# Performance work log

Hardware: AMD Instinct MI355X
Metric: run time of the kernel (lower is better)

Reference implementation:

```python
import jax, jax.numpy as jnp
import numpy as np
from jax import lax

B, V_ECC, V_ERR, T, C = 8192, 16, 12, 25, 32
F_IN = C * T           # 800 = temporal_out * tf_num
G = 64                 # gcn_out
H2 = 256               # hidden_size * 2
EHR_DIM, EHR_OUT = 64, 64

def _lhat(V):
    # bidirectional ring graph; PyG ChebConv sym-norm with lambda_max=2.0:
    # L_hat = (2/lmax) * (I - D^-1/2 A D^-1/2) - I = -D^-1/2 A D^-1/2
    i = np.arange(V)
    src = np.concatenate([i, (i + 1) % V])
    dst = np.concatenate([(i + 1) % V, i])
    A = np.zeros((V, V), np.float32)
    A[src, dst] = 1.0
    deg = A.sum(1)
    dinv = np.where(deg > 0, deg ** -0.5, 0.0).astype(np.float32)
    return jnp.asarray(-(dinv[:, None] * A * dinv[None, :]))

LHAT_ECC = _lhat(V_ECC)
LHAT_ERR = _lhat(V_ERR)

def setup_inputs():
    key = jax.random.key(0)
    ks = jax.random.split(key, 23)
    n = lambda k, s: jax.random.normal(k, s, jnp.float32) * 0.02
    return {
        "ecc": jax.random.normal(ks[0], (B, V_ECC, T), jnp.float32),
        "err": jax.random.normal(ks[1], (B, V_ERR, T), jnp.float32),
        "ehr": jax.random.normal(ks[2], (B, EHR_DIM), jnp.float32),
        "wt_ecc": n(ks[3], (C, 1, 3)), "bt_ecc": n(ks[4], (C,)),
        "wt_err": n(ks[5], (C, 1, 3)), "bt_err": n(ks[6], (C,)),
        "W0_ecc": n(ks[7], (F_IN, G)), "W1_ecc": n(ks[8], (F_IN, G)), "b_ecc": n(ks[9], (G,)),
        "W0_err": n(ks[10], (F_IN, G)), "W1_err": n(ks[11], (F_IN, G)), "b_err": n(ks[12], (G,)),
        "Wp_ecc": n(ks[13], (V_ECC * G, H2)), "bp_ecc": n(ks[14], (H2,)),
        "Wp_err": n(ks[15], (V_ERR * G, H2)), "bp_err": n(ks[16], (H2,)),
        "Wa": n(ks[17], (H2, 1)), "ba": n(ks[18], (1,)),
        "We": n(ks[19], (EHR_DIM, EHR_OUT)), "be": n(ks[20], (EHR_OUT,)),
        "Wf2": n(ks[21], (H2 + EHR_OUT, 1)), "bf2": n(ks[22], (1,)),
    }

def _temporal(x, w, b):
    # x: [B, V, T]; Conv1d(1 -> C, k=3, padding=1) per node, then flatten (C, T)
    bb, v, t = x.shape
    y = lax.conv_general_dilated(x.reshape(bb * v, 1, t), w, (1,), "SAME",
                                 dimension_numbers=("NCH", "OIH", "NCH"))
    y = y + b[None, :, None]
    return y.reshape(bb, v, -1)        # [B, V, C*T]

def _cheb(x, lhat, w0, w1, b):
    # K=2 ChebConv: out = T0(x)@W0 + T1(x)@W1 + b, T1 = L_hat x (batched over B)
    tx1 = jnp.einsum("uv,bvd->bud", lhat, x)
    return x @ w0 + tx1 @ w1 + b

def reference(ecc, err, ehr, wt_ecc, bt_ecc, wt_err, bt_err,
              W0_ecc, W1_ecc, b_ecc, W0_err, W1_err, b_err,
              Wp_ecc, bp_ecc, Wp_err, bp_err, Wa, ba, We, be, Wf2, bf2):
    bsz = ecc.shape[0]
    ecc_f = _temporal(ecc, wt_ecc, bt_ecc)                    # [B,16,800]
    err_f = _temporal(err, wt_err, bt_err)                    # [B,12,800]
    ecc_out = _cheb(ecc_f, LHAT_ECC, W0_ecc, W1_ecc, b_ecc)   # [B,16,64]
    err_out = _cheb(err_f, LHAT_ERR, W0_err, W1_err, b_err)   # [B,12,64]
    ecc_g = ecc_out.reshape(bsz, -1) @ Wp_ecc + bp_ecc        # [B,256]
    err_g = err_out.reshape(bsz, -1) @ Wp_err + bp_err        # [B,256]
    attn = jax.nn.sigmoid(jnp.tanh(ecc_g + err_g) @ Wa + ba)  # [B,1]
    fused = attn * ecc_g + (1.0 - attn) * err_g
    ehr_p = jax.nn.relu(ehr @ We + be)                        # dropout = identity (eval)
    combined = jnp.concatenate([fused, ehr_p], axis=1)        # [B,320]
    x = jax.nn.relu(combined)
    return jax.nn.sigmoid(x @ Wf2 + bf2)                      # [B,1]
```

## Files before the change

### kernel.cpp

```cpp
#include <hip/hip_runtime.h>
#include <math.h>

#define B_TOT 8192
#define KE 400
#define KR 300
#define MEP 416
#define MRP 320

#define ROWS 16

#define SXE_LD 424
#define SXR_LD 328
#define SEH_LD 72

#define OFF_WEFF0E 0
#define OFF_WEFF1E 1600
#define OFF_WEFF0R 3200
#define OFF_WEFF1R 4800
#define OFF_CVE    6400
#define OFF_CVR    6464
#define OFF_BE     6528
#define OFF_BR     6784
#define U_AET 14080
#define U_ART (U_AET + 256 * MEP)
#define U_WET (U_ART + 256 * MRP)

typedef __attribute__((ext_vector_type(8))) short short8;
typedef __attribute__((ext_vector_type(4))) float floatx4;

__device__ __forceinline__ float sigmoidf_(float x) { return 1.f / (1.f + __expf(-x)); }
__device__ __forceinline__ float tanhf_(float x) { float e = __expf(2.f * x); return (e - 1.f) / (e + 1.f); }
__device__ __forceinline__ unsigned short f2bf(float x) {
    unsigned u = __float_as_uint(x);
    u += 0x7fffu + ((u >> 16) & 1u);
    return (unsigned short)(u >> 16);
}

__global__ __launch_bounds__(256) void fold_temporal(
    const float* __restrict__ wt_ecc, const float* __restrict__ bt_ecc,
    const float* __restrict__ wt_err, const float* __restrict__ bt_err,
    const float* __restrict__ W0_ecc, const float* __restrict__ W1_ecc, const float* __restrict__ b_ecc,
    const float* __restrict__ W0_err, const float* __restrict__ W1_err, const float* __restrict__ b_err,
    float* __restrict__ ws)
{
    const int blk = blockIdx.x;
    const int tid = threadIdx.x;
    const int cq = tid >> 6;
    const int g  = tid & 63;

    __shared__ float red[4][64];

    if (blk < 100) {
        const int m = blk / 25;
        const int tin = blk % 25;
        const bool is_err = (m >= 2);
        const float* wt = is_err ? wt_err : wt_ecc;
        const float* W = (m & 1) ? (is_err ? W1_err : W1_ecc) : (is_err ? W0_err : W0_ecc);
        const int t0 = tin > 0 ? tin - 1 : 0;
        const int t1 = tin < 24 ? tin + 1 : 24;
        float s = 0.f;
        #pragma unroll
        for (int c8 = 0; c8 < 8; ++c8) {
            const int c = cq * 8 + c8;
            for (int t = t0; t <= t1; ++t) {
                const int k = tin - t + 1;
                s = fmaf(wt[c * 3 + k], W[(c * 25 + t) * 64 + g], s);
            }
        }
        red[cq][g] = s;
        __syncthreads();
        if (tid < 64)
            ws[m * 1600 + tin * 64 + g] = red[0][g] + red[1][g] + red[2][g] + red[3][g];
    } else if (blk < 102) {
        const bool is_err = (blk == 101);
        const float* bt = is_err ? bt_err : bt_ecc;
        const float* W0 = is_err ? W0_err : W0_ecc;
        const float* W1 = is_err ? W1_err : W1_ecc;
        const float* bb = is_err ? b_err : b_ecc;
        float s = 0.f;
        #pragma unroll
        for (int c8 = 0; c8 < 8; ++c8) {
            const int c = cq * 8 + c8;
            const float btc = bt[c];
            #pragma unroll
            for (int t = 0; t < 25; ++t) {
                const int ct = (c * 25 + t) * 64 + g;
                s = fmaf(btc, W0[ct] - W1[ct], s);
            }
        }
        red[cq][g] = s;
        __syncthreads();
        if (tid < 64)
            ws[(is_err ? OFF_CVR : OFF_CVE) + g] =
                bb[g] + red[0][g] + red[1][g] + red[2][g] + red[3][g];
    } else {
        ws[OFF_BE + tid] = 0.f;
        ws[OFF_BR + tid] = 0.f;
    }
}

__global__ __launch_bounds__(256) void fold_graph(
    const float* __restrict__ Wp_ecc, const float* __restrict__ bp_ecc,
    const float* __restrict__ Wp_err, const float* __restrict__ bp_err,
    const float* __restrict__ We,
    float* __restrict__ wsf, unsigned short* __restrict__ wsu)
{
    const int blk = blockIdx.x;
    const int h = threadIdx.x;

    if (blk < MEP) {
        const int k = blk;
        float s = 0.f;
        if (k < KE) {
            const int v = k / 25, tin = k % 25;
            const int vp = (v + 1) & 15, vm = (v + 15) & 15;
            const float* w0 = wsf + OFF_WEFF0E + tin * 64;
            const float* w1 = wsf + OFF_WEFF1E + tin * 64;
            #pragma unroll 4
            for (int g = 0; g < 64; ++g) {
                s = fmaf(w0[g], Wp_ecc[(v * 64 + g) * 256 + h], s);
                s = fmaf(-0.5f * w1[g], Wp_ecc[(vp * 64 + g) * 256 + h] + Wp_ecc[(vm * 64 + g) * 256 + h], s);
            }
        }
        wsu[U_AET + (size_t)h * MEP + k] = f2bf(s);
    } else if (blk < MEP + MRP) {
        const int k = blk - MEP;
        float s = 0.f;
        if (k < KR) {
            const int v = k / 25, tin = k % 25;
            const int vp = (v + 1) % 12, vm = (v + 11) % 12;
            const float* w0 = wsf + OFF_WEFF0R + tin * 64;
            const float* w1 = wsf + OFF_WEFF1R + tin * 64;
            #pragma unroll 4
            for (int g = 0; g < 64; ++g) {
                s = fmaf(w0[g], Wp_err[(v * 64 + g) * 256 + h], s);
                s = fmaf(-0.5f * w1[g], Wp_err[(vp * 64 + g) * 256 + h] + Wp_err[(vm * 64 + g) * 256 + h], s);
            }
        }
        wsu[U_ART + (size_t)h * MRP + k] = f2bf(s);
    } else if (blk < MEP + MRP + 16) {
        const int i = blk - (MEP + MRP);
        const float* cv = wsf + OFF_CVE;
        float s = (i == 0) ? bp_ecc[h] : 0.f;
        #pragma unroll 4
        for (int jj = 0; jj < 64; ++jj) {
            const int j = i * 64 + jj;
            s = fmaf(cv[j & 63], Wp_ecc[(size_t)j * 256 + h], s);
        }
        atomicAdd(&wsf[OFF_BE + h], s);
    } else if (blk < MEP + MRP + 32) {
        const int i = blk - (MEP + MRP + 16);
        const float* cv = wsf + OFF_CVR;
        float s = (i == 0) ? bp_err[h] : 0.f;
        if (i < 12) {
            #pragma unroll 4
            for (int jj = 0; jj < 64; ++jj) {
                const int j = i * 64 + jj;
                s = fmaf(cv[j & 63], Wp_err[(size_t)j * 256 + h], s);
            }
        }
        atomicAdd(&wsf[OFF_BR + h], s);
    } else {
        for (int it = 0; it < 16; ++it) {
            const int idx = it * 256 + h;
            const int e = idx >> 6, d = idx & 63;
            wsu[U_WET + e * 64 + d] = f2bf(We[d * 64 + e]);
        }
    }
}

__global__ __launch_bounds__(256, 3) void fused_main(
    const float* __restrict__ ecc, const float* __restrict__ err, const float* __restrict__ ehr,
    const float* __restrict__ wsf, const unsigned short* __restrict__ wsu,
    const float* __restrict__ Wa, const float* __restrict__ ba,
    const float* __restrict__ be_, const float* __restrict__ Wf2, const float* __restrict__ bf2,
    float* __restrict__ out)
{
    const unsigned short* awt_e = wsu + U_AET;
    const unsigned short* awt_r = wsu + U_ART;
    const unsigned short* wet   = wsu + U_WET;
    const float* biasE = wsf + OFF_BE;
    const float* biasR = wsf + OFF_BR;

    __shared__ __align__(16) char smem[ROWS * SXE_LD * 2 + ROWS * SXR_LD * 2 + ROWS * SEH_LD * 2];
    unsigned short* sxe = (unsigned short*)smem;
    unsigned short* sxr = sxe + ROWS * SXE_LD;
    unsigned short* seh = sxr + ROWS * SXR_LD;
    float* pa_part = (float*)smem;
    float* at_arr  = pa_part + 64;
    float* po_part = at_arr + 16;

    const int tid = threadIdx.x;
    const int row0 = blockIdx.x * ROWS;

    for (int it = 0; it < 7; ++it) {
        const int f = it * 256 + tid;
        if (f < ROWS * 106) {
            const int r = f / 106, q = f - r * 106;
            float4 v = make_float4(0.f, 0.f, 0.f, 0.f);
            if (q < 100) v = *(const float4*)(ecc + (size_t)(row0 + r) * KE + q * 4);
            const unsigned p0 = (unsigned)f2bf(v.x) | ((unsigned)f2bf(v.y) << 16);
            const unsigned p1 = (unsigned)f2bf(v.z) | ((unsigned)f2bf(v.w) << 16);
            *(uint2*)&sxe[r * SXE_LD + q * 4] = make_uint2(p0, p1);
        }
    }
    for (int it = 0; it < 6; ++it) {
        const int f = it * 256 + tid;
        if (f < ROWS * 82) {
            const int r = f / 82, q = f - r * 82;
            float4 v = make_float4(0.f, 0.f, 0.f, 0.f);
            if (q < 75) v = *(const float4*)(err + (size_t)(row0 + r) * KR + q * 4);
            const unsigned p0 = (unsigned)f2bf(v.x) | ((unsigned)f2bf(v.y) << 16);
            const unsigned p1 = (unsigned)f2bf(v.z) | ((unsigned)f2bf(v.w) << 16);
            *(uint2*)&sxr[r * SXR_LD + q * 4] = make_uint2(p0, p1);
        }
    }
    {
        const int r = tid >> 4, q = tid & 15;
        const float4 v = *(const float4*)(ehr + (size_t)(row0 + r) * 64 + q * 4);
        const unsigned p0 = (unsigned)f2bf(v.x) | ((unsigned)f2bf(v.y) << 16);
        const unsigned p1 = (unsigned)f2bf(v.z) | ((unsigned)f2bf(v.w) << 16);
        *(uint2*)&seh[r * SEH_LD + q * 4] = make_uint2(p0, p1);
    }
    __syncthreads();

    const int wv = tid >> 6, lane = tid & 63;
    const int lm = lane & 15, lq = lane >> 4;
    const int n0 = wv * 64;

    floatx4 accE[4], accR[4], accH;
    accH = (floatx4){0.f, 0.f, 0.f, 0.f};
    #pragma unroll
    for (int nt = 0; nt < 4; ++nt) {
        accE[nt] = (floatx4){0.f, 0.f, 0.f, 0.f};
        accR[nt] = (floatx4){0.f, 0.f, 0.f, 0.f};
    }

    #pragma unroll
    for (int kc = 0; kc < 2; ++kc) {
        const short8 b = *(const short8*)(wet + (wv * 16 + lm) * 64 + kc * 32 + lq * 8);
        const short8 a = *(const short8*)&seh[lm * SEH_LD + kc * 32 + lq * 8];
        accH = __builtin_amdgcn_mfma_f32_16x16x32_bf16(a, b, accH, 0, 0, 0);
    }
    #pragma unroll
    for (int kc = 0; kc < 13; ++kc) {
        const short8 a0 = *(const short8*)&sxe[lm * SXE_LD + kc * 32 + lq * 8];
        #pragma unroll
        for (int nt = 0; nt < 4; ++nt) {
            const short8 b = *(const short8*)(awt_e + (size_t)(n0 + nt * 16 + lm) * MEP + kc * 32 + lq * 8);
            accE[nt] = __builtin_amdgcn_mfma_f32_16x16x32_bf16(a0, b, accE[nt], 0, 0, 0);
        }
    }
    #pragma unroll
    for (int kc = 0; kc < 10; ++kc) {
        const short8 a0 = *(const short8*)&sxr[lm * SXR_LD + kc * 32 + lq * 8];
        #pragma unroll
        for (int nt = 0; nt < 4; ++nt) {
            const short8 b = *(const short8*)(awt_r + (size_t)(n0 + nt * 16 + lm) * MRP + kc * 32 + lq * 8);
            accR[nt] = __builtin_amdgcn_mfma_f32_16x16x32_bf16(a0, b, accR[nt], 0, 0, 0);
        }
    }

    float bE[4], bR[4], wa[4], wf[4];
    #pragma unroll
    for (int nt = 0; nt < 4; ++nt) {
        const int h = n0 + nt * 16 + lm;
        bE[nt] = biasE[h]; bR[nt] = biasR[h]; wa[nt] = Wa[h]; wf[nt] = Wf2[h];
    }
    const int e_lane = wv * 16 + lm;
    const float eh_be = be_[e_lane];
    const float eh_wf = Wf2[256 + e_lane];

    float pa_lane[4];
    #pragma unroll
    for (int rg = 0; rg < 4; ++rg) {
        float s = 0.f;
        #pragma unroll
        for (int nt = 0; nt < 4; ++nt) {
            const float ev = accE[nt][rg] + bE[nt];
            const float rv = accR[nt][rg] + bR[nt];
            s = fmaf(tanhf_(ev + rv), wa[nt], s);
        }
        s += __shfl_xor(s, 1, 64); s += __shfl_xor(s, 2, 64);
        s += __shfl_xor(s, 4, 64); s += __shfl_xor(s, 8, 64);
        pa_lane[rg] = s;
    }

    __syncthreads();
    if (lm == 0) {
        #pragma unroll
        for (int rg = 0; rg < 4; ++rg)
            pa_part[wv * 16 + lq * 4 + rg] = pa_lane[rg];
    }
    __syncthreads();
    if (tid < 16)
        at_arr[tid] = sigmoidf_(pa_part[tid] + pa_part[16 + tid] + pa_part[32 + tid] + pa_part[48 + tid] + ba[0]);
    __syncthreads();

    float po_lane[4];
    #pragma unroll
    for (int rg = 0; rg < 4; ++rg) {
        const int r = lq * 4 + rg;
        const float at = at_arr[r];
        const float om = 1.f - at;
        float s = 0.f;
        #pragma unroll
        for (int nt = 0; nt < 4; ++nt) {
            const float ev = accE[nt][rg] + bE[nt];
            const float rv = accR[nt][rg] + bR[nt];
            s = fmaf(fmaxf(at * ev + om * rv, 0.f), wf[nt], s);
        }
        s = fmaf(fmaxf(accH[rg] + eh_be, 0.f), eh_wf, s);
        s += __shfl_xor(s, 1, 64); s += __shfl_xor(s, 2, 64);
        s += __shfl_xor(s, 4, 64); s += __shfl_xor(s, 8, 64);
        po_lane[rg] = s;
    }
    if (lm == 0) {
        #pragma unroll
        for (int rg = 0; rg < 4; ++rg)
            po_part[wv * 16 + lq * 4 + rg] = po_lane[rg];
    }
    __syncthreads();
    if (tid < 16)
        out[row0 + tid] = sigmoidf_(po_part[tid] + po_part[16 + tid] + po_part[32 + tid] + po_part[48 + tid] + bf2[0]);
}

extern "C" void kernel_launch(void* const* d_in, const int* in_sizes, int n_in,
                              void* d_out, int out_size, void* d_ws, size_t ws_size,
                              hipStream_t stream)
{
    (void)in_sizes; (void)n_in; (void)out_size; (void)ws_size;
    const float* ecc    = (const float*)d_in[0];
    const float* err    = (const float*)d_in[1];
    const float* ehr    = (const float*)d_in[2];
    const float* wt_ecc = (const float*)d_in[3];
    const float* bt_ecc = (const float*)d_in[4];
    const float* wt_err = (const float*)d_in[5];
    const float* bt_err = (const float*)d_in[6];
    const float* W0_ecc = (const float*)d_in[7];
    const float* W1_ecc = (const float*)d_in[8];
    const float* b_ecc  = (const float*)d_in[9];
    const float* W0_err = (const float*)d_in[10];
    const float* W1_err = (const float*)d_in[11];
    const float* b_err  = (const float*)d_in[12];
    const float* Wp_ecc = (const float*)d_in[13];
    const float* bp_ecc = (const float*)d_in[14];
    const float* Wp_err = (const float*)d_in[15];
    const float* bp_err = (const float*)d_in[16];
    const float* Wa     = (const float*)d_in[17];
    const float* ba     = (const float*)d_in[18];
    const float* We     = (const float*)d_in[19];
    const float* be     = (const float*)d_in[20];
    const float* Wf2    = (const float*)d_in[21];
    const float* bf2    = (const float*)d_in[22];
    float* wsf = (float*)d_ws;
    unsigned short* wsu = (unsigned short*)d_ws;
    float* out = (float*)d_out;

    fold_temporal<<<dim3(103), dim3(256), 0, stream>>>(
        wt_ecc, bt_ecc, wt_err, bt_err, W0_ecc, W1_ecc, b_ecc, W0_err, W1_err, b_err, wsf);
    fold_graph<<<dim3(MEP + MRP + 32 + 1), dim3(256), 0, stream>>>(
        Wp_ecc, bp_ecc, Wp_err, bp_err, We, wsf, wsu);
    fused_main<<<dim3(B_TOT / ROWS), dim3(256), 0, stream>>>(
        ecc, err, ehr, wsf, wsu, Wa, ba, be, Wf2, bf2, out);
}
```

Before: 147.0 us.

## Merge the two weight-folding kernels into one launch with recomputed temporal folds

Fuses fold_temporal and fold_graph into a single fold_all kernel. Each graph-fold block now recomputes its own temporal-folded W0/W1 row in shared memory, and two blocks compute the bias vectors directly instead of using atomics. This removes one kernel launch and the dependency between the two launches, at the cost of redundant temporal-fold work across blocks. It also raises fused_main's launch_bounds minimum blocks from 3 to 4, which may cap registers.

```diff
diff --git a/kernel.cpp b/kernel.cpp
--- a/kernel.cpp
+++ b/kernel.cpp
@@ -13,14 +13,8 @@
 #define SXR_LD 328
 #define SEH_LD 72
 
-#define OFF_WEFF0E 0
-#define OFF_WEFF1E 1600
-#define OFF_WEFF0R 3200
-#define OFF_WEFF1R 4800
-#define OFF_CVE    6400
-#define OFF_CVR    6464
-#define OFF_BE     6528
-#define OFF_BR     6784
+#define OFF_BE 6528
+#define OFF_BR 6784
 #define U_AET 14080
 #define U_ART (U_AET + 256 * MEP)
 #define U_WET (U_ART + 256 * MRP)
@@ -36,47 +30,35 @@
     return (unsigned short)(u >> 16);
 }
 
-__global__ __launch_bounds__(256) void fold_temporal(
+__global__ __launch_bounds__(256) void fold_all(
     const float* __restrict__ wt_ecc, const float* __restrict__ bt_ecc,
     const float* __restrict__ wt_err, const float* __restrict__ bt_err,
     const float* __restrict__ W0_ecc, const float* __restrict__ W1_ecc, const float* __restrict__ b_ecc,
     const float* __restrict__ W0_err, const float* __restrict__ W1_err, const float* __restrict__ b_err,
-    float* __restrict__ ws)
+    const float* __restrict__ Wp_ecc, const float* __restrict__ bp_ecc,
+    const float* __restrict__ Wp_err, const float* __restrict__ bp_err,
+    const float* __restrict__ We,
+    float* __restrict__ wsf, unsigned short* __restrict__ wsu)
 {
     const int blk = blockIdx.x;
     const int tid = threadIdx.x;
     const int cq = tid >> 6;
     const int g  = tid & 63;
 
-    __shared__ float red[4][64];
-
-    if (blk < 100) {
-        const int m = blk / 25;
-        const int tin = blk % 25;
-        const bool is_err = (m >= 2);
-        const float* wt = is_err ? wt_err : wt_ecc;
-        const float* W = (m & 1) ? (is_err ? W1_err : W1_ecc) : (is_err ? W0_err : W0_ecc);
-        const int t0 = tin > 0 ? tin - 1 : 0;
-        const int t1 = tin < 24 ? tin + 1 : 24;
-        float s = 0.f;
-        #pragma unroll
-        for (int c8 = 0; c8 < 8; ++c8) {
-            const int c = cq * 8 + c8;
-            for (int t = t0; t <= t1; ++t) {
-                const int k = tin - t + 1;
-                s = fmaf(wt[c * 3 + k], W[(c * 25 + t) * 64 + g], s);
-            }
-        }
-        red[cq][g] = s;
-        __syncthreads();
-        if (tid < 64)
-            ws[m * 1600 + tin * 64 + g] = red[0][g] + red[1][g] + red[2][g] + red[3][g];
-    } else if (blk < 102) {
-        const bool is_err = (blk == 101);
+    __shared__ float red0[4][64];
+    __shared__ float red1[4][64];
+    __shared__ float sw0[64];
+    __shared__ float sw1[64];
+
+    if (blk < 2) {
+        const bool is_err = (blk == 1);
         const float* bt = is_err ? bt_err : bt_ecc;
         const float* W0 = is_err ? W0_err : W0_ecc;
         const float* W1 = is_err ? W1_err : W1_ecc;
         const float* bb = is_err ? b_err : b_ecc;
+        const float* Wp = is_err ? Wp_err : Wp_ecc;
+        const float* bp = is_err ? bp_err : bp_ecc;
+        const int J = (is_err ? 12 : 16) * 64;
         float s = 0.f;
         #pragma unroll
         for (int c8 = 0; c8 < 8; ++c8) {
@@ -88,88 +70,79 @@
                 s = fmaf(btc, W0[ct] - W1[ct], s);
             }
         }
-        red[cq][g] = s;
+        red0[cq][g] = s;
         __syncthreads();
         if (tid < 64)
-            ws[(is_err ? OFF_CVR : OFF_CVE) + g] =
-                bb[g] + red[0][g] + red[1][g] + red[2][g] + red[3][g];
-    } else {
-        ws[OFF_BE + tid] = 0.f;
-        ws[OFF_BR + tid] = 0.f;
-    }
-}
-
-__global__ __launch_bounds__(256) void fold_graph(
-    const float* __restrict__ Wp_ecc, const float* __restrict__ bp_ecc,
-    const float* __restrict__ Wp_err, const float* __restrict__ bp_err,
-    const float* __restrict__ We,
-    float* __restrict__ wsf, unsigned short* __restrict__ wsu)
-{
-    const int blk = blockIdx.x;
-    const int h = threadIdx.x;
-
-    if (blk < MEP) {
-        const int k = blk;
-        float s = 0.f;
-        if (k < KE) {
-            const int v = k / 25, tin = k % 25;
-            const int vp = (v + 1) & 15, vm = (v + 15) & 15;
-            const float* w0 = wsf + OFF_WEFF0E + tin * 64;
-            const float* w1 = wsf + OFF_WEFF1E + tin * 64;
-            #pragma unroll 4
-            for (int g = 0; g < 64; ++g) {
-                s = fmaf(w0[g], Wp_ecc[(v * 64 + g) * 256 + h], s);
-                s = fmaf(-0.5f * w1[g], Wp_ecc[(vp * 64 + g) * 256 + h] + Wp_ecc[(vm * 64 + g) * 256 + h], s);
-            }
-        }
-        wsu[U_AET + (size_t)h * MEP + k] = f2bf(s);
-    } else if (blk < MEP + MRP) {
-        const int k = blk - MEP;
-        float s = 0.f;
-        if (k < KR) {
-            const int v = k / 25, tin = k % 25;
-            const int vp = (v + 1) % 12, vm = (v + 11) % 12;
-            const float* w0 = wsf + OFF_WEFF0R + tin * 64;
-            const float* w1 = wsf + OFF_WEFF1R + tin * 64;
-            #pragma unroll 4
-            for (int g = 0; g < 64; ++g) {
-                s = fmaf(w0[g], Wp_err[(v * 64 + g) * 256 + h], s);
-                s = fmaf(-0.5f * w1[g], Wp_err[(vp * 64 + g) * 256 + h] + Wp_err[(vm * 64 + g) * 256 + h], s);
-            }
-        }
-        wsu[U_ART + (size_t)h * MRP + k] = f2bf(s);
-    } else if (blk < MEP + MRP + 16) {
-        const int i = blk - (MEP + MRP);
-        const float* cv = wsf + OFF_CVE;
-        float s = (i == 0) ? bp_ecc[h] : 0.f;
-        #pragma unroll 4
-        for (int jj = 0; jj < 64; ++jj) {
-            const int j = i * 64 + jj;
-            s = fmaf(cv[j & 63], Wp_ecc[(size_t)j * 256 + h], s);
-        }
-        atomicAdd(&wsf[OFF_BE + h], s);
-    } else if (blk < MEP + MRP + 32) {
-        const int i = blk - (MEP + MRP + 16);
-        const float* cv = wsf + OFF_CVR;
-        float s = (i == 0) ? bp_err[h] : 0.f;
-        if (i < 12) {
-            #pragma unroll 4
-            for (int jj = 0; jj < 64; ++jj) {
-                const int j = i * 64 + jj;
-                s = fmaf(cv[j & 63], Wp_err[(size_t)j * 256 + h], s);
-            }
-        }
-        atomicAdd(&wsf[OFF_BR + h], s);
-    } else {
+            sw0[g] = bb[g] + red0[0][g] + red0[1][g] + red0[2][g] + red0[3][g];
+        __syncthreads();
+        const int h = tid;
+        float a0 = 0.f, a1 = 0.f, a2 = 0.f, a3 = 0.f;
+        for (int j = 0; j < J; j += 4) {
+            a0 = fmaf(sw0[(j + 0) & 63], Wp[(size_t)(j + 0) * 256 + h], a0);
+            a1 = fmaf(sw0[(j + 1) & 63], Wp[(size_t)(j + 1) * 256 + h], a1);
+            a2 = fmaf(sw0[(j + 2) & 63], Wp[(size_t)(j + 2) * 256 + h], a2);
+            a3 = fmaf(sw0[(j + 3) & 63], Wp[(size_t)(j + 3) * 256 + h], a3);
+        }
+        wsf[(is_err ? OFF_BR : OFF_BE) + h] = bp[h] + ((a0 + a1) + (a2 + a3));
+    } else if (blk == 2) {
         for (int it = 0; it < 16; ++it) {
-            const int idx = it * 256 + h;
+            const int idx = it * 256 + tid;
             const int e = idx >> 6, d = idx & 63;
             wsu[U_WET + e * 64 + d] = f2bf(We[d * 64 + e]);
         }
+    } else {
+        const int kb = blk - 3;
+        const bool is_err = (kb >= MEP);
+        const int k  = is_err ? kb - MEP : kb;
+        const int KK = is_err ? KR : KE;
+        const int MP = is_err ? MRP : MEP;
+        const float* wt = is_err ? wt_err : wt_ecc;
+        const float* W0 = is_err ? W0_err : W0_ecc;
+        const float* W1 = is_err ? W1_err : W1_ecc;
+        const float* Wp = is_err ? Wp_err : Wp_ecc;
+        const int ubase = is_err ? U_ART : U_AET;
+
+        float s = 0.f;
+        if (k < KK) {
+            const int v = k / 25, tin = k % 25;
+            const int t0 = tin > 0 ? tin - 1 : 0;
+            const int t1 = tin < 24 ? tin + 1 : 24;
+            float s0 = 0.f, s1 = 0.f;
+            #pragma unroll
+            for (int c8 = 0; c8 < 8; ++c8) {
+                const int c = cq * 8 + c8;
+                for (int t = t0; t <= t1; ++t) {
+                    const int kk = tin - t + 1;
+                    const float w = wt[c * 3 + kk];
+                    const int ct = (c * 25 + t) * 64 + g;
+                    s0 = fmaf(w, W0[ct], s0);
+                    s1 = fmaf(w, W1[ct], s1);
+                }
+            }
+            red0[cq][g] = s0;
+            red1[cq][g] = s1;
+            __syncthreads();
+            if (tid < 64)
+                sw0[g] = red0[0][g] + red0[1][g] + red0[2][g] + red0[3][g];
+            else if (tid < 128)
+                sw1[tid - 64] = red1[0][tid - 64] + red1[1][tid - 64] + red1[2][tid - 64] + red1[3][tid - 64];
+            __syncthreads();
+
+            const int nv = is_err ? 12 : 16;
+            const int vp = (v + 1) % nv;
+            const int vm = (v + nv - 1) % nv;
+            const int h = tid;
+            #pragma unroll 4
+            for (int gg = 0; gg < 64; ++gg) {
+                s = fmaf(sw0[gg], Wp[(v * 64 + gg) * 256 + h], s);
+                s = fmaf(-0.5f * sw1[gg], Wp[(vp * 64 + gg) * 256 + h] + Wp[(vm * 64 + gg) * 256 + h], s);
+            }
+        }
+        wsu[ubase + (size_t)tid * MP + k] = f2bf(s);
     }
 }
 
-__global__ __launch_bounds__(256, 3) void fused_main(
+__global__ __launch_bounds__(256, 4) void fused_main(
     const float* __restrict__ ecc, const float* __restrict__ err, const float* __restrict__ ehr,
     const float* __restrict__ wsf, const unsigned short* __restrict__ wsu,
     const float* __restrict__ Wa, const float* __restrict__ ba,
@@ -357,9 +330,9 @@
     unsigned short* wsu = (unsigned short*)d_ws;
     float* out = (float*)d_out;
 
-    fold_temporal<<<dim3(103), dim3(256), 0, stream>>>(
-        wt_ecc, bt_ecc, wt_err, bt_err, W0_ecc, W1_ecc, b_ecc, W0_err, W1_err, b_err, wsf);
-    fold_graph<<<dim3(MEP + MRP + 32 + 1), dim3(256), 0, stream>>>(
+    fold_all<<<dim3(3 + MEP + MRP), dim3(256), 0, stream>>>(
+        wt_ecc, bt_ecc, wt_err, bt_err,
+        W0_ecc, W1_ecc, b_ecc, W0_err, W1_err, b_err,
         Wp_ecc, bp_ecc, Wp_err, bp_err, We, wsf, wsu);
     fused_main<<<dim3(B_TOT / ROWS), dim3(256), 0, stream>>>(
         ecc, err, ehr, wsf, wsu, Wa, ba, be, Wf2, bf2, out);
```

Result: slower. 168.6 us (+14.7%).

## Pre-convert activations to bf16 in fold kernel and drop shared-memory staging

Applied to the files above, without the earlier changes.

Moves the fp32-to-bf16 conversion of the ecc/err/ehr inputs out of the main kernel into extra blocks of the fold_graph launch, which write padded bf16 copies to the workspace. The main kernel then loads MFMA A-operands straight from global memory, with no LDS staging and no barrier. This shrinks LDS use and removes the conversion prologue from the main kernel. The cost is an extra full write and re-read of the activations through global memory, roughly 1.3x the input bytes on top of the original read.

```diff
diff --git a/kernel.cpp b/kernel.cpp
--- a/kernel.cpp
+++ b/kernel.cpp
@@ -8,10 +8,6 @@
 #define MRP 320
 
 #define ROWS 16
-
-#define SXE_LD 424
-#define SXR_LD 328
-#define SEH_LD 72
 
 #define OFF_WEFF0E 0
 #define OFF_WEFF1E 1600
@@ -24,6 +20,14 @@
 #define U_AET 14080
 #define U_ART (U_AET + 256 * MEP)
 #define U_WET (U_ART + 256 * MRP)
+#define U_XE  (U_WET + 64 * 64)
+#define U_XR  (U_XE + 8192 * MEP)
+#define U_XH  (U_XR + 8192 * MRP)
+
+#define TCE (8192 * 52)
+#define TCR (8192 * 40)
+#define TCH (8192 * 8)
+#define CONVB 768
 
 typedef __attribute__((ext_vector_type(8))) short short8;
 typedef __attribute__((ext_vector_type(4))) float floatx4;
@@ -34,6 +38,14 @@
     unsigned u = __float_as_uint(x);
     u += 0x7fffu + ((u >> 16) & 1u);
     return (unsigned short)(u >> 16);
+}
+__device__ __forceinline__ uint4 pack8(float4 a, float4 b) {
+    uint4 r;
+    r.x = (unsigned)f2bf(a.x) | ((unsigned)f2bf(a.y) << 16);
+    r.y = (unsigned)f2bf(a.z) | ((unsigned)f2bf(a.w) << 16);
+    r.z = (unsigned)f2bf(b.x) | ((unsigned)f2bf(b.y) << 16);
+    r.w = (unsigned)f2bf(b.z) | ((unsigned)f2bf(b.w) << 16);
+    return r;
 }
 
 __global__ __launch_bounds__(256) void fold_temporal(
@@ -103,6 +115,7 @@
     const float* __restrict__ Wp_ecc, const float* __restrict__ bp_ecc,
     const float* __restrict__ Wp_err, const float* __restrict__ bp_err,
     const float* __restrict__ We,
+    const float* __restrict__ ecc, const float* __restrict__ err, const float* __restrict__ ehr,
     float* __restrict__ wsf, unsigned short* __restrict__ wsu)
 {
     const int blk = blockIdx.x;
@@ -160,17 +173,52 @@
             }
         }
         atomicAdd(&wsf[OFF_BR + h], s);
-    } else {
+    } else if (blk < MEP + MRP + 33) {
         for (int it = 0; it < 16; ++it) {
             const int idx = it * 256 + h;
             const int e = idx >> 6, d = idx & 63;
             wsu[U_WET + e * 64 + d] = f2bf(We[d * 64 + e]);
         }
+    } else {
+        const int cb = blk - (MEP + MRP + 33);
+        const float4 z4 = make_float4(0.f, 0.f, 0.f, 0.f);
+        for (int idx = cb * 256 + h; idx < TCE + TCR + TCH; idx += CONVB * 256) {
+            if (idx < TCE) {
+                const int row = idx / 52, c8 = idx - row * 52;
+                uint4 o;
+                if (c8 < 50) {
+                    const float* p = ecc + (size_t)row * KE + c8 * 8;
+                    o = pack8(*(const float4*)p, *(const float4*)(p + 4));
+                } else {
+                    o = make_uint4(0u, 0u, 0u, 0u);
+                }
+                *(uint4*)(wsu + U_XE + (size_t)row * MEP + c8 * 8) = o;
+            } else if (idx < TCE + TCR) {
+                const int j = idx - TCE;
+                const int row = j / 40, c8 = j - row * 40;
+                uint4 o;
+                if (c8 < 37) {
+                    const float* p = err + (size_t)row * KR + c8 * 8;
+                    o = pack8(*(const float4*)p, *(const float4*)(p + 4));
+                } else if (c8 == 37) {
+                    const float* p = err + (size_t)row * KR + 296;
+                    o = pack8(*(const float4*)p, z4);
+                } else {
+                    o = make_uint4(0u, 0u, 0u, 0u);
+                }
+                *(uint4*)(wsu + U_XR + (size_t)row * MRP + c8 * 8) = o;
+            } else {
+                const int j = idx - TCE - TCR;
+                const int row = j >> 3, c8 = j & 7;
+                const float* p = ehr + (size_t)row * 64 + c8 * 8;
+                *(uint4*)(wsu + U_XH + (size_t)row * 64 + c8 * 8) =
+                    pack8(*(const float4*)p, *(const float4*)(p + 4));
+            }
+        }
     }
 }
 
 __global__ __launch_bounds__(256, 3) void fused_main(
-    const float* __restrict__ ecc, const float* __restrict__ err, const float* __restrict__ ehr,
     const float* __restrict__ wsf, const unsigned short* __restrict__ wsu,
     const float* __restrict__ Wa, const float* __restrict__ ba,
     const float* __restrict__ be_, const float* __restrict__ Wf2, const float* __restrict__ bf2,
@@ -182,52 +230,20 @@
     const float* biasE = wsf + OFF_BE;
     const float* biasR = wsf + OFF_BR;
 
-    __shared__ __align__(16) char smem[ROWS * SXE_LD * 2 + ROWS * SXR_LD * 2 + ROWS * SEH_LD * 2];
-    unsigned short* sxe = (unsigned short*)smem;
-    unsigned short* sxr = sxe + ROWS * SXE_LD;
-    unsigned short* seh = sxr + ROWS * SXR_LD;
-    float* pa_part = (float*)smem;
-    float* at_arr  = pa_part + 64;
-    float* po_part = at_arr + 16;
+    __shared__ float pa_part[64];
+    __shared__ float at_arr[16];
+    __shared__ float po_part[64];
 
     const int tid = threadIdx.x;
     const int row0 = blockIdx.x * ROWS;
-
-    for (int it = 0; it < 7; ++it) {
-        const int f = it * 256 + tid;
-        if (f < ROWS * 106) {
-            const int r = f / 106, q = f - r * 106;
-            float4 v = make_float4(0.f, 0.f, 0.f, 0.f);
-            if (q < 100) v = *(const float4*)(ecc + (size_t)(row0 + r) * KE + q * 4);
-            const unsigned p0 = (unsigned)f2bf(v.x) | ((unsigned)f2bf(v.y) << 16);
-            const unsigned p1 = (unsigned)f2bf(v.z) | ((unsigned)f2bf(v.w) << 16);
-            *(uint2*)&sxe[r * SXE_LD + q * 4] = make_uint2(p0, p1);
-        }
-    }
-    for (int it = 0; it < 6; ++it) {
-        const int f = it * 256 + tid;
-        if (f < ROWS * 82) {
-            const int r = f / 82, q = f - r * 82;
-            float4 v = make_float4(0.f, 0.f, 0.f, 0.f);
-            if (q < 75) v = *(const float4*)(err + (size_t)(row0 + r) * KR + q * 4);
-            const unsigned p0 = (unsigned)f2bf(v.x) | ((unsigned)f2bf(v.y) << 16);
-            const unsigned p1 = (unsigned)f2bf(v.z) | ((unsigned)f2bf(v.w) << 16);
-            *(uint2*)&sxr[r * SXR_LD + q * 4] = make_uint2(p0, p1);
-        }
-    }
-    {
-        const int r = tid >> 4, q = tid & 15;
-        const float4 v = *(const float4*)(ehr + (size_t)(row0 + r) * 64 + q * 4);
-        const unsigned p0 = (unsigned)f2bf(v.x) | ((unsigned)f2bf(v.y) << 16);
-        const unsigned p1 = (unsigned)f2bf(v.z) | ((unsigned)f2bf(v.w) << 16);
-        *(uint2*)&seh[r * SEH_LD + q * 4] = make_uint2(p0, p1);
-    }
-    __syncthreads();
-
     const int wv = tid >> 6, lane = tid & 63;
     const int lm = lane & 15, lq = lane >> 4;
     const int n0 = wv * 64;
 
+    const unsigned short* xe = wsu + U_XE + (size_t)(row0 + lm) * MEP + lq * 8;
+    const unsigned short* xr = wsu + U_XR + (size_t)(row0 + lm) * MRP + lq * 8;
+    const unsigned short* xh = wsu + U_XH + (size_t)(row0 + lm) * 64  + lq * 8;
+
     floatx4 accE[4], accR[4], accH;
     accH = (floatx4){0.f, 0.f, 0.f, 0.f};
     #pragma unroll
@@ -239,12 +255,12 @@
     #pragma unroll
     for (int kc = 0; kc < 2; ++kc) {
         const short8 b = *(const short8*)(wet + (wv * 16 + lm) * 64 + kc * 32 + lq * 8);
-        const short8 a = *(const short8*)&seh[lm * SEH_LD + kc * 32 + lq * 8];
+        const short8 a = *(const short8*)(xh + kc * 32);
         accH = __builtin_amdgcn_mfma_f32_16x16x32_bf16(a, b, accH, 0, 0, 0);
     }
     #pragma unroll
     for (int kc = 0; kc < 13; ++kc) {
-        const short8 a0 = *(const short8*)&sxe[lm * SXE_LD + kc * 32 + lq * 8];
+        const short8 a0 = *(const short8*)(xe + kc * 32);
         #pragma unroll
         for (int nt = 0; nt < 4; ++nt) {
             const short8 b = *(const short8*)(awt_e + (size_t)(n0 + nt * 16 + lm) * MEP + kc * 32 + lq * 8);
@@ -253,7 +269,7 @@
     }
     #pragma unroll
     for (int kc = 0; kc < 10; ++kc) {
-        const short8 a0 = *(const short8*)&sxr[lm * SXR_LD + kc * 32 + lq * 8];
+        const short8 a0 = *(const short8*)(xr + kc * 32);
         #pragma unroll
         for (int nt = 0; nt < 4; ++nt) {
             const short8 b = *(const short8*)(awt_r + (size_t)(n0 + nt * 16 + lm) * MRP + kc * 32 + lq * 8);
@@ -264,8 +280,8 @@
     float bE[4], bR[4], wa[4], wf[4];
     #pragma unroll
     for (int nt = 0; nt < 4; ++nt) {
-        const int h = n0 + nt * 16 + lm;
-        bE[nt] = biasE[h]; bR[nt] = biasR[h]; wa[nt] = Wa[h]; wf[nt] = Wf2[h];
+        const int hh = n0 + nt * 16 + lm;
+        bE[nt] = biasE[hh]; bR[nt] = biasR[hh]; wa[nt] = Wa[hh]; wf[nt] = Wf2[hh];
     }
     const int e_lane = wv * 16 + lm;
     const float eh_be = be_[e_lane];
@@ -286,7 +302,6 @@
         pa_lane[rg] = s;
     }
 
-    __syncthreads();
     if (lm == 0) {
         #pragma unroll
         for (int rg = 0; rg < 4; ++rg)
@@ -359,8 +374,8 @@
 
     fold_temporal<<<dim3(103), dim3(256), 0, stream>>>(
         wt_ecc, bt_ecc, wt_err, bt_err, W0_ecc, W1_ecc, b_ecc, W0_err, W1_err, b_err, wsf);
-    fold_graph<<<dim3(MEP + MRP + 32 + 1), dim3(256), 0, stream>>>(
-        Wp_ecc, bp_ecc, Wp_err, bp_err, We, wsf, wsu);
+    fold_graph<<<dim3(MEP + MRP + 33 + CONVB), dim3(256), 0, stream>>>(
+        Wp_ecc, bp_ecc, Wp_err, bp_err, We, ecc, err, ehr, wsf, wsu);
     fused_main<<<dim3(B_TOT / ROWS), dim3(256), 0, stream>>>(
-        ecc, err, ehr, wsf, wsu, Wa, ba, be, Wf2, bf2, out);
-}
+        wsf, wsu, Wa, ba, be, Wf2, bf2, out);
+}
```

Result: slower. 152.9 us (+4.0%).

## Restructure graph-weight folding to reuse Wp rows across time steps per block

Applied to the files above, without the earlier changes.

The fold_graph kernel now assigns one node and half of the time steps to each block instead of one (node, time) pair. Each thread loads its Wp rows into registers and reuses them across 13 time steps. This cuts the redundant global reads of Wp and the block count from 769 to 85. Padding columns are now zeroed explicitly by the last block. The trade-off is far fewer blocks, so less GPU parallelism, and longer per-thread work.

```diff
diff --git a/kernel.cpp b/kernel.cpp
--- a/kernel.cpp
+++ b/kernel.cpp
@@ -108,38 +108,52 @@
     const int blk = blockIdx.x;
     const int h = threadIdx.x;
 
-    if (blk < MEP) {
-        const int k = blk;
-        float s = 0.f;
-        if (k < KE) {
-            const int v = k / 25, tin = k % 25;
-            const int vp = (v + 1) & 15, vm = (v + 15) & 15;
-            const float* w0 = wsf + OFF_WEFF0E + tin * 64;
-            const float* w1 = wsf + OFF_WEFF1E + tin * 64;
-            #pragma unroll 4
-            for (int g = 0; g < 64; ++g) {
-                s = fmaf(w0[g], Wp_ecc[(v * 64 + g) * 256 + h], s);
-                s = fmaf(-0.5f * w1[g], Wp_ecc[(vp * 64 + g) * 256 + h] + Wp_ecc[(vm * 64 + g) * 256 + h], s);
+    if (blk < 56) {
+        const bool is_err = (blk >= 32);
+        const int b = is_err ? blk - 32 : blk;
+        const int v = b >> 1, half = b & 1;
+        const int t0 = half * 13;
+        const int nv = is_err ? 12 : 16;
+        const int MP = is_err ? MRP : MEP;
+        const float* Wp = is_err ? Wp_err : Wp_ecc;
+        const float* w0 = wsf + (is_err ? OFF_WEFF0R : OFF_WEFF0E);
+        const float* w1 = wsf + (is_err ? OFF_WEFF1R : OFF_WEFF1E);
+        const int ubase = is_err ? U_ART : U_AET;
+        const int vp = (v + 1) % nv;
+        const int vm = (v + nv - 1) % nv;
+
+        float acc[13];
+        #pragma unroll
+        for (int tt = 0; tt < 13; ++tt) acc[tt] = 0.f;
+
+        for (int gc = 0; gc < 64; gc += 16) {
+            float p0[16], pp[16], pm[16];
+            #pragma unroll
+            for (int i = 0; i < 16; ++i) {
+                const int g = gc + i;
+                p0[i] = Wp[(v  * 64 + g) * 256 + h];
+                pp[i] = Wp[(vp * 64 + g) * 256 + h];
+                pm[i] = Wp[(vm * 64 + g) * 256 + h];
             }
-        }
-        wsu[U_AET + (size_t)h * MEP + k] = f2bf(s);
-    } else if (blk < MEP + MRP) {
-        const int k = blk - MEP;
-        float s = 0.f;
-        if (k < KR) {
-            const int v = k / 25, tin = k % 25;
-            const int vp = (v + 1) % 12, vm = (v + 11) % 12;
-            const float* w0 = wsf + OFF_WEFF0R + tin * 64;
-            const float* w1 = wsf + OFF_WEFF1R + tin * 64;
-            #pragma unroll 4
-            for (int g = 0; g < 64; ++g) {
-                s = fmaf(w0[g], Wp_err[(v * 64 + g) * 256 + h], s);
-                s = fmaf(-0.5f * w1[g], Wp_err[(vp * 64 + g) * 256 + h] + Wp_err[(vm * 64 + g) * 256 + h], s);
+            #pragma unroll
+            for (int tt = 0; tt < 13; ++tt) {
+                const int tin = t0 + tt;
+                #pragma unroll
+                for (int i = 0; i < 16; ++i) {
+                    const int g = gc + i;
+                    acc[tt] = fmaf(w0[tin * 64 + g], p0[i], acc[tt]);
+                    acc[tt] = fmaf(-0.5f * w1[tin * 64 + g], pp[i] + pm[i], acc[tt]);
+                }
             }
         }
-        wsu[U_ART + (size_t)h * MRP + k] = f2bf(s);
-    } else if (blk < MEP + MRP + 16) {
-        const int i = blk - (MEP + MRP);
+        #pragma unroll
+        for (int tt = 0; tt < 13; ++tt) {
+            const int tin = t0 + tt;
+            if (tin < 25)
+                wsu[ubase + (size_t)h * MP + v * 25 + tin] = f2bf(acc[tt]);
+        }
+    } else if (blk < 72) {
+        const int i = blk - 56;
         const float* cv = wsf + OFF_CVE;
         float s = (i == 0) ? bp_ecc[h] : 0.f;
         #pragma unroll 4
@@ -148,16 +162,14 @@
             s = fmaf(cv[j & 63], Wp_ecc[(size_t)j * 256 + h], s);
         }
         atomicAdd(&wsf[OFF_BE + h], s);
-    } else if (blk < MEP + MRP + 32) {
-        const int i = blk - (MEP + MRP + 16);
+    } else if (blk < 84) {
+        const int i = blk - 72;
         const float* cv = wsf + OFF_CVR;
         float s = (i == 0) ? bp_err[h] : 0.f;
-        if (i < 12) {
-            #pragma unroll 4
-            for (int jj = 0; jj < 64; ++jj) {
-                const int j = i * 64 + jj;
-                s = fmaf(cv[j & 63], Wp_err[(size_t)j * 256 + h], s);
-            }
+        #pragma unroll 4
+        for (int jj = 0; jj < 64; ++jj) {
+            const int j = i * 64 + jj;
+            s = fmaf(cv[j & 63], Wp_err[(size_t)j * 256 + h], s);
         }
         atomicAdd(&wsf[OFF_BR + h], s);
     } else {
@@ -165,6 +177,17 @@
             const int idx = it * 256 + h;
             const int e = idx >> 6, d = idx & 63;
             wsu[U_WET + e * 64 + d] = f2bf(We[d * 64 + e]);
+        }
+        {
+            const uint4 z = make_uint4(0u, 0u, 0u, 0u);
+            *(uint4*)(wsu + U_AET + (size_t)h * MEP + 400) = z;
+            *(uint4*)(wsu + U_AET + (size_t)h * MEP + 408) = z;
+        }
+        {
+            const uint2 z2 = make_uint2(0u, 0u);
+            #pragma unroll
+            for (int q = 0; q < 5; ++q)
+                *(uint2*)(wsu + U_ART + (size_t)h * MRP + 300 + q * 4) = z2;
         }
     }
 }
@@ -359,7 +382,7 @@
 
     fold_temporal<<<dim3(103), dim3(256), 0, stream>>>(
         wt_ecc, bt_ecc, wt_err, bt_err, W0_ecc, W1_ecc, b_ecc, W0_err, W1_err, b_err, wsf);
-    fold_graph<<<dim3(MEP + MRP + 32 + 1), dim3(256), 0, stream>>>(
+    fold_graph<<<dim3(85), dim3(256), 0, stream>>>(
         Wp_ecc, bp_ecc, Wp_err, bp_err, We, wsf, wsu);
     fused_main<<<dim3(B_TOT / ROWS), dim3(256), 0, stream>>>(
         ecc, err, ehr, wsf, wsu, Wa, ba, be, Wf2, bf2, out);
```

Result: slower. 169.7 us (+15.5%).
